# Performance work log

Measured on AMD Instinct MI355X. Metric: run time of the kernel, lower is better.

Reference implementation:

```python
import jax, jax.numpy as jnp
import numpy as np

NUM_CLASSES = 80
C_OUT = 81
SCORE_THR = 0.02
IOU_THR = 0.45
TOPK = 1000
IMG_MAX = 320.0
STRIDES = [16, 32, 64, 107, 160, 320]
MIN_SIZES = [48, 100, 150, 202, 253, 304]
MAX_SIZES = [100, 150, 202, 253, 304, 320]
FEAT = [20, 10, 5, 3, 2, 1]
MAX_RATIO = float(abs(np.log(0.016)))


def _base_anchors(level):
    base = float(MIN_SIZES[level])
    scales = np.array([1.0, np.sqrt(MAX_SIZES[level] / MIN_SIZES[level])])
    ratios = np.array([1.0, 0.5, 2.0, 1.0 / 3.0, 3.0])
    h_ratios = np.sqrt(ratios)
    w_ratios = 1.0 / h_ratios
    # scale_major=False: scales vary along rows
    ws = (base * scales[:, None] * w_ratios[None, :]).reshape(-1)
    hs = (base * scales[:, None] * h_ratios[None, :]).reshape(-1)
    c = STRIDES[level] / 2.0
    ba = np.stack([c - 0.5 * ws, c - 0.5 * hs, c + 0.5 * ws, c + 0.5 * hs], -1)
    return ba[[0, 5, 1, 2, 3, 4]]  # index_select reorder, 6 anchors/loc


def _priors(level):
    ba = _base_anchors(level)
    f, s = FEAT[level], STRIDES[level]
    sx = np.arange(f, dtype=np.float64) * s
    xx = np.tile(sx, f)
    yy = np.repeat(sx, f)
    shifts = np.stack([xx, yy, xx, yy], -1)  # [f*f,4]
    return (ba[None, :, :] + shifts[:, None, :]).reshape(-1, 4).astype(np.float32)


PRIORS = [jnp.asarray(_priors(i)) for i in range(6)]


def delta2bbox(priors, deltas):
    stds = jnp.array([0.1, 0.1, 0.2, 0.2], dtype=deltas.dtype)
    d = deltas * stds
    pxy = (priors[:, :2] + priors[:, 2:]) * 0.5
    pwh = priors[:, 2:] - priors[:, :2]
    dwh = jnp.clip(d[:, 2:], -MAX_RATIO, MAX_RATIO)
    gxy = pxy + pwh * d[:, :2]
    gwh = pwh * jnp.exp(dwh)
    boxes = jnp.concatenate([gxy - 0.5 * gwh, gxy + 0.5 * gwh], -1)
    return jnp.clip(boxes, 0.0, IMG_MAX)


def _nms_keep(boxes, valid, iou_thr):
    # greedy NMS over score-sorted boxes; returns bool keep mask
    K = boxes.shape[0]
    area = (boxes[:, 2] - boxes[:, 0]) * (boxes[:, 3] - boxes[:, 1])
    lt = jnp.maximum(boxes[:, None, :2], boxes[None, :, :2])
    rb = jnp.minimum(boxes[:, None, 2:], boxes[None, :, 2:])
    wh = jnp.clip(rb - lt, 0.0)
    inter = wh[..., 0] * wh[..., 1]
    iou = inter / (area[:, None] + area[None, :] - inter)
    ar = jnp.arange(K)

    def body(i, alive):
        sup = (iou[i] > iou_thr) & (ar > i) & alive[i]
        return alive & ~sup

    return jax.lax.fori_loop(0, K, body, valid)


def _single_image(cls_list, bb_list):
    boxes_l, scores_l, labels_l, valid_l = [], [], [], []
    for cls, bb, priors in zip(cls_list, bb_list, PRIORS):
        probs = jax.nn.softmax(cls.transpose(1, 2, 0).reshape(-1, C_OUT), axis=-1)[:, :NUM_CLASSES]
        flat = probs.reshape(-1)  # [N*80]
        k = min(TOPK, flat.shape[0])
        masked = jnp.where(flat > SCORE_THR, flat, -1.0)
        vals, idx = jax.lax.top_k(masked, k)
        valid = vals > SCORE_THR
        a_idx = idx // NUM_CLASSES
        lbl = idx % NUM_CLASSES
        deltas = bb.transpose(1, 2, 0).reshape(-1, 4)[a_idx]
        boxes = delta2bbox(priors[a_idx], deltas)
        boxes_l.append(boxes)
        scores_l.append(jnp.where(valid, vals, 0.0))
        labels_l.append(lbl)
        valid_l.append(valid)
    boxes = jnp.concatenate(boxes_l, 0)   # [K,4]
    scores = jnp.concatenate(scores_l, 0)
    labels = jnp.concatenate(labels_l, 0)
    valid = jnp.concatenate(valid_l, 0)

    # batched (class-aware) NMS via per-class coordinate offsets
    max_coord = boxes.max()
    offsets = labels.astype(boxes.dtype) * (max_coord + 1.0)
    boxes_nms = boxes + offsets[:, None]
    order = jnp.argsort(-jnp.where(valid, scores, -jnp.inf))
    boxes_s = boxes[order]
    scores_s = scores[order]
    labels_s = labels[order]
    valid_s = valid[order]
    keep = jax.lax.stop_gradient(
        _nms_keep(jax.lax.stop_gradient(boxes_nms[order]), valid_s, IOU_THR))
    dets = jnp.concatenate([boxes_s, scores_s[:, None]], -1) * keep[:, None].astype(boxes.dtype)
    return dets, labels_s, keep


def setup_inputs() -> dict:
    key = jax.random.key(0)
    ks = jax.random.split(key, 12)
    B = 4
    inp = {}
    for i, f in enumerate(FEAT):
        inp[f"cls{i}"] = jax.random.normal(ks[i], (B, 486, f, f), dtype=jnp.float32)
        inp[f"bb{i}"] = jax.random.normal(ks[6 + i], (B, 24, f, f), dtype=jnp.float32)
    return inp


def reference(cls0, cls1, cls2, cls3, cls4, cls5, bb0, bb1, bb2, bb3, bb4, bb5):
    def one(c0, c1, c2, c3, c4, c5, b0, b1, b2, b3, b4, b5):
        return _single_image([c0, c1, c2, c3, c4, c5], [b0, b1, b2, b3, b4, b5])
    dets, labels, keep = jax.vmap(one)(cls0, cls1, cls2, cls3, cls4, cls5,
                                       bb0, bb1, bb2, bb3, bb4, bb5)
    return dets, labels, keep
```

## Files before the change

kernel.cpp:

```cpp
#include <hip/hip_runtime.h>
#include <stdint.h>

#define NB 4
#define KTOT 5480
#define PER_IMG 258720
#define SCORE_THR 0.02f
#define IOU_THR 0.45f
#define REL_BASE 0x3CA3D70Bu
#define JCH 10
#define JSZ 548
#define ICH 11
#define NMSCAP 512

__constant__ int cFEAT[6]    = {20,10,5,3,2,1};
__constant__ int cSTRIDE[6]  = {16,32,64,107,160,320};
__constant__ int cMIN[6]     = {48,100,150,202,253,304};
__constant__ int cMAX[6]     = {100,150,202,253,304,320};
__constant__ int cNFLAT[6]   = {192000,48000,12000,4320,1920,480};
__constant__ int cFLATOFF[6] = {0,192000,240000,252000,256320,258240};
__constant__ int cKSEL[6]    = {1000,1000,1000,1000,1000,480};
__constant__ int cKOFF[6]    = {0,1000,2000,3000,4000,5000};
__constant__ double cRATIO[6] = {1.0,1.0,0.5,2.0,1.0/3.0,3.0};
__constant__ int eTLEV[14]   = {0,0,0,0,0,0,0,0,1,1,2,3,4,5};
__constant__ int eTCHK[14]   = {0,1,2,3,4,5,6,7,0,1,0,0,0,0};
__constant__ int eNCH[6]     = {8,2,1,1,1,1};

__device__ __forceinline__ unsigned long long mk_key(unsigned kb, int lev, unsigned idx) {
  return ((unsigned long long)kb << 21) |
         (unsigned long long)(0x1FFFFFu ^ (((unsigned)lev << 18) | idx));
}

__device__ __forceinline__ unsigned long long shfl64(unsigned long long x, int src) {
  int lo = __shfl((int)(unsigned)(x & 0xffffffffull), src);
  int hi = __shfl((int)(unsigned)(x >> 32), src);
  return ((unsigned long long)(unsigned)hi << 32) | (unsigned)lo;
}

__global__ __launch_bounds__(256) void k_softmax(
    const float* __restrict__ c0, const float* __restrict__ c1,
    const float* __restrict__ c2, const float* __restrict__ c3,
    const float* __restrict__ c4, const float* __restrict__ c5,
    float* __restrict__ scores, unsigned* __restrict__ ghist)
{
  int t = blockIdx.x;
  int b = t / 78, rem = t % 78;
  int lev, a, cb;
  if (rem < 42)      { lev = 0; a = rem / 7;        cb = (rem % 7) * 64; }
  else if (rem < 54) { lev = 1; a = (rem - 42) >> 1; cb = ((rem - 42) & 1) * 64; }
  else               { lev = 2 + (rem - 54) / 6; a = (rem - 54) % 6; cb = 0; }
  const float* cls = (lev==0)?c0:(lev==1)?c1:(lev==2)?c2:(lev==3)?c3:(lev==4)?c4:c5;
  int f = cFEAT[lev], ff = f * f;
  int ncell = ff - cb; if (ncell > 64) ncell = 64;

  __shared__ float tile[81 * 64];
  const float* base = cls + (size_t)(b * 486 + a * 81) * ff + cb;
  for (int t2 = threadIdx.x; t2 < 81 * 64; t2 += 256) {
    int c = t2 >> 6, cell = t2 & 63;
    if (cell < ncell)
      tile[(c << 6) | (cell ^ (c & 63))] = base[c * ff + cell];
  }
  __syncthreads();

  int lane = threadIdx.x & 63, w = threadIdx.x >> 6;
  unsigned* h = ghist + (size_t)(b * 6 + lev) * 8192;
  for (int cell = w; cell < ncell; cell += 4) {
    float v1 = tile[(lane << 6) | (cell ^ lane)];
    float v2 = (lane <= 16) ? tile[((lane + 64) << 6) | (cell ^ lane)]
                            : __uint_as_float(0xff800000u);
    float mx = fmaxf(v1, v2);
    #pragma unroll
    for (int m = 32; m; m >>= 1) mx = fmaxf(mx, __shfl_xor(mx, m));
    float e1 = expf(v1 - mx);
    float e2 = (lane <= 16) ? expf(v2 - mx) : 0.f;
    float sm = e1 + e2;
    #pragma unroll
    for (int m = 32; m; m >>= 1) sm += __shfl_xor(sm, m);
    int row = (cb + cell) * 6 + a;
    float* out = scores + (size_t)b * PER_IMG + cFLATOFF[lev] + row * 80;
    float p1 = e1 / sm;
    out[lane] = (p1 > SCORE_THR) ? p1 : -1.f;
    if (p1 > SCORE_THR)
      atomicAdd(&h[(__float_as_uint(p1) - REL_BASE) >> 13], 1u);
    if (lane < 16) {
      float p2 = e2 / sm;
      out[lane + 64] = (p2 > SCORE_THR) ? p2 : -1.f;
      if (p2 > SCORE_THR)
        atomicAdd(&h[(__float_as_uint(p2) - REL_BASE) >> 13], 1u);
    }
  }
}

__global__ __launch_bounds__(1024) void k_plan(
    const unsigned* __restrict__ ghist, unsigned* __restrict__ ctrl)
{
  int task = blockIdx.x;
  int lev = task % 6;
  int tid = threadIdx.x;
  if (lev == 5) { if (tid == 0) ctrl[task * 8] = 2u; return; }
  unsigned k = (unsigned)cKSEL[lev];
  const unsigned* h = ghist + (size_t)task * 8192;
  unsigned loc[8];
  unsigned ssum = 0;
  #pragma unroll
  for (int j = 0; j < 8; ++j) { loc[j] = h[tid * 8 + j]; ssum += loc[j]; }
  __shared__ unsigned sc[1024];
  sc[tid] = ssum;
  __syncthreads();
  for (int off = 1; off < 1024; off <<= 1) {
    unsigned cur = sc[tid];
    unsigned add = (tid + off < 1024) ? sc[tid + off] : 0u;
    __syncthreads();
    sc[tid] = cur + add;
    __syncthreads();
  }
  unsigned c = sc[0];
  if (c < k) { if (tid == 0) ctrl[task * 8] = 1u; return; }
  unsigned above = (tid == 1023) ? 0u : sc[tid + 1];
  unsigned run = above;
  #pragma unroll
  for (int j = 7; j >= 0; --j) {
    unsigned hj = loc[j];
    if (run < k && run + hj >= k) {
      ctrl[task * 8 + 0] = 0u;
      ctrl[task * 8 + 1] = (unsigned)(tid * 8 + j);
    }
    run += hj;
  }
}

__global__ __launch_bounds__(256) void k_emit2(
    const float* __restrict__ scores, unsigned* __restrict__ ctrl,
    unsigned long long* __restrict__ selkeys, unsigned long long* __restrict__ eqg)
{
  int b = blockIdx.x / 14, ent = blockIdx.x % 14;
  int lev = eTLEV[ent], chk = eTCHK[ent];
  int task = b * 6 + lev;
  int n = cNFLAT[lev];
  int tid = threadIdx.x;
  const float* s = scores + (size_t)b * PER_IMG + cFLATOFF[lev];
  unsigned long long* out = selkeys + (size_t)b * KTOT + cKOFF[lev];

  if (lev == 5) {
    for (int i = tid; i < n; i += 256) {
      float v = s[i];
      unsigned kb = (v > SCORE_THR) ? __float_as_uint(v) : 0u;
      out[i] = mk_key(kb, lev, (unsigned)i);
    }
    return;
  }

  __shared__ unsigned long long wbuf[1024];
  __shared__ unsigned long long ebuf[4096];
  __shared__ unsigned wcnt, ecnt, sbw, sbe;
  if (tid == 0) { wcnt = 0; ecnt = 0; }
  __syncthreads();

  unsigned mode = ctrl[task * 8];
  int csz = n / eNCH[lev];
  int start = chk * csz;
  const float4* s4 = (const float4*)(s + start);
  int n4 = csz >> 2;

  if (mode == 0u) {
    unsigned b1 = ctrl[task * 8 + 1];
    unsigned base_lo = REL_BASE + (b1 << 13);
    unsigned base_hi = base_lo + 8192u;
    #pragma unroll 4
    for (int i0 = tid; i0 < n4; i0 += 256) {
      float4 vv = s4[i0];
      #pragma unroll
      for (int e2 = 0; e2 < 4; ++e2) {
        float v = (e2==0)?vv.x:(e2==1)?vv.y:(e2==2)?vv.z:vv.w;
        if (v > SCORE_THR) {
          unsigned kb = __float_as_uint(v);
          unsigned idx = (unsigned)(start + i0 * 4 + e2);
          if (kb >= base_hi) {
            unsigned p = atomicAdd(&wcnt, 1u);
            if (p < 1024u) wbuf[p] = mk_key(kb, lev, idx);
          } else if (kb >= base_lo) {
            unsigned p = atomicAdd(&ecnt, 1u);
            if (p < 4096u) ebuf[p] = mk_key(kb, lev, idx);
          }
        }
      }
    }
  } else {
    #pragma unroll 4
    for (int i0 = tid; i0 < n4; i0 += 256) {
      float4 vv = s4[i0];
      #pragma unroll
      for (int e2 = 0; e2 < 4; ++e2) {
        float v = (e2==0)?vv.x:(e2==1)?vv.y:(e2==2)?vv.z:vv.w;
        if (v > SCORE_THR) {
          unsigned p = atomicAdd(&wcnt, 1u);
          if (p < 1024u) wbuf[p] = mk_key(__float_as_uint(v), lev,
                                          (unsigned)(start + i0 * 4 + e2));
        }
      }
    }
  }
  __syncthreads();
  if (tid == 0) {
    sbw = atomicAdd(&ctrl[task * 8 + 2], wcnt);
    sbe = atomicAdd(&ctrl[task * 8 + 3], ecnt);
  }
  __syncthreads();
  unsigned nw = (wcnt < 1024u) ? wcnt : 1024u;
  unsigned ne = (ecnt < 4096u) ? ecnt : 4096u;
  unsigned bw = sbw, be = sbe;
  for (unsigned t = tid; t < nw; t += 256) out[bw + t] = wbuf[t];
  for (unsigned t = tid; t < ne; t += 256) {
    unsigned g = be + t;
    if (g < 4096u) eqg[(size_t)task * 4096 + g] = ebuf[t];
  }
}

__global__ __launch_bounds__(1024) void k_finalize2(
    const float* __restrict__ scores, const unsigned* __restrict__ ctrl,
    unsigned long long* __restrict__ selkeys, const unsigned long long* __restrict__ eqg)
{
  int task = blockIdx.x;
  int b = task / 6, lev = task % 6;
  if (lev == 5) return;
  int tid = threadIdx.x;
  unsigned k = (unsigned)cKSEL[lev];
  int n = cNFLAT[lev];
  const float* s = scores + (size_t)b * PER_IMG + cFLATOFF[lev];
  unsigned long long* out = selkeys + (size_t)b * KTOT + cKOFF[lev];
  unsigned levtag = (unsigned)lev << 18;
  unsigned mode = ctrl[task * 8];

  __shared__ unsigned long long eqb[4096];
  __shared__ unsigned sc[1024];
  __shared__ unsigned sh_cnt, sh_eq, sh_byte, sh_r;

  if (mode == 0u) {
    unsigned cnt = ctrl[task * 8 + 2];
    unsigned e = ctrl[task * 8 + 3];
    unsigned need = k - cnt;
    if (e <= 4096u) {
      const unsigned long long* eq = eqg + (size_t)task * 4096;
      if (e == need) {
        for (unsigned t = tid; t < need; t += 1024) out[cnt + t] = eq[t];
        return;
      }
      unsigned P = 1; while (P < e) P <<= 1;
      for (unsigned t = tid; t < P; t += 1024) eqb[t] = (t < e) ? eq[t] : 0ull;
      __syncthreads();
      for (unsigned sz = 2; sz <= P; sz <<= 1)
        for (unsigned st = sz >> 1; st; st >>= 1) {
          for (unsigned w = tid; w < P / 2; w += 1024) {
            unsigned i = ((w & ~(st - 1)) << 1) | (w & (st - 1));
            unsigned l = i | st;
            bool up = ((i & sz) == 0);
            unsigned long long A = eqb[i], B = eqb[l];
            if ((A < B) == up) { eqb[i] = B; eqb[l] = A; }
          }
          __syncthreads();
        }
      for (unsigned t = tid; t < need; t += 1024) out[cnt + t] = eqb[t];
      return;
    }
  } else if (mode == 1u) {
    unsigned c = ctrl[task * 8 + 2];
    unsigned need = k - c;
    unsigned base = 0;
    for (int start = 0; start < n && base < need; start += 1024) {
      int i = start + tid;
      unsigned pred = (i < n && !(s[i] > SCORE_THR)) ? 1u : 0u;
      sc[tid] = pred;
      __syncthreads();
      for (int off = 1; off < 1024; off <<= 1) {
        unsigned add = (tid >= off) ? sc[tid - off] : 0u;
        unsigned v = sc[tid];
        __syncthreads();
        sc[tid] = v + add;
        __syncthreads();
      }
      unsigned incl = sc[tid];
      unsigned total = sc[1023];
      unsigned excl = incl - pred;
      if (pred && (base + excl) < need)
        out[c + base + excl] =
            (unsigned long long)(0x1FFFFFu ^ (levtag | (unsigned)i));
      __syncthreads();
      base += total;
    }
    return;
  }

  unsigned* hist = sc;
  unsigned* equ = (unsigned*)eqb;
  unsigned prefix = 0, r = k;
  for (int pass = 3; pass >= 0; --pass) {
    int shift = pass * 8;
    for (int i = tid; i < 256; i += 1024) hist[i] = 0;
    __syncthreads();
    for (int i = tid; i < n; i += 1024) {
      float v = s[i];
      unsigned kb = (v > SCORE_THR) ? __float_as_uint(v) : 0u;
      bool match = (pass == 3) || (((kb ^ prefix) >> (shift + 8)) == 0u);
      if (match) atomicAdd(&hist[(kb >> shift) & 255u], 1u);
    }
    __syncthreads();
    if (tid == 0) {
      unsigned cum = 0, byte = 0, rr = r;
      for (int bb = 255; bb >= 0; --bb) {
        unsigned hh = hist[bb];
        if (cum + hh >= r) { byte = (unsigned)bb; rr = r - cum; break; }
        cum += hh;
      }
      sh_byte = byte; sh_r = rr;
    }
    __syncthreads();
    prefix |= (sh_byte << shift);
    r = sh_r;
    __syncthreads();
  }
  unsigned Kstar = prefix;
  if (tid == 0) { sh_cnt = 0; sh_eq = 0; }
  __syncthreads();
  for (int i = tid; i < n; i += 1024) {
    float v = s[i];
    unsigned kb = (v > SCORE_THR) ? __float_as_uint(v) : 0u;
    if (kb > Kstar) {
      unsigned slot = atomicAdd(&sh_cnt, 1u);
      out[slot] = mk_key(kb, lev, (unsigned)i);
    } else if (kb == Kstar) {
      unsigned es = atomicAdd(&sh_eq, 1u);
      if (es < 4096u) equ[es] = (unsigned)i;
    }
  }
  __syncthreads();
  unsigned m = sh_cnt;
  unsigned e2 = (sh_eq < 4096u) ? sh_eq : 4096u;
  unsigned need2 = k - m;
  if (e2 > need2) {
    unsigned P = 1; while (P < e2) P <<= 1;
    for (unsigned t = tid; t < P; t += 1024) if (t >= e2) equ[t] = 0xFFFFFFFFu;
    __syncthreads();
    for (unsigned sz = 2; sz <= P; sz <<= 1)
      for (unsigned st = sz >> 1; st; st >>= 1) {
        for (unsigned w = tid; w < P / 2; w += 1024) {
          unsigned i = ((w & ~(st - 1)) << 1) | (w & (st - 1));
          unsigned l = i | st;
          bool up = ((i & sz) == 0);
          unsigned A = equ[i], B = equ[l];
          if ((A > B) == up) { equ[i] = B; equ[l] = A; }
        }
        __syncthreads();
      }
  }
  __syncthreads();
  for (unsigned t = tid; t < need2; t += 1024)
    out[m + t] = ((unsigned long long)Kstar << 21) |
                 (unsigned long long)(0x1FFFFFu ^ (levtag | equ[t]));
}

__global__ __launch_bounds__(512) void k_rank(
    const unsigned long long* __restrict__ selkeys, unsigned* __restrict__ rank_part)
{
  int blk = blockIdx.x;
  int jc = blk % JCH;
  int rest = blk / JCH;
  int ic = rest % ICH, b = rest / ICH;
  int tid = threadIdx.x;
  __shared__ __align__(16) unsigned long long sk[JSZ];
  const unsigned long long* keys = selkeys + (size_t)b * KTOT;
  for (int j = tid; j < JSZ; j += 512) sk[j] = keys[jc * JSZ + j];
  int i = ic * 512 + tid;
  unsigned long long mk = (i < KTOT) ? keys[i] : 0ull;
  __syncthreads();
  unsigned r = 0;
  const ulonglong2* sk2 = (const ulonglong2*)sk;
  #pragma unroll 8
  for (int j = 0; j < JSZ / 2; ++j) {
    ulonglong2 kk = sk2[j];
    r += (kk.x > mk) ? 1u : 0u;
    r += (kk.y > mk) ? 1u : 0u;
  }
  if (i < KTOT) rank_part[((size_t)jc * NB + b) * KTOT + i] = r;
}

__global__ __launch_bounds__(512) void k_decode(
    const unsigned long long* __restrict__ selkeys, const unsigned* __restrict__ rank_part,
    const float* __restrict__ g0, const float* __restrict__ g1,
    const float* __restrict__ g2, const float* __restrict__ g3,
    const float* __restrict__ g4, const float* __restrict__ g5,
    float* __restrict__ boxes, float* __restrict__ oscore,
    unsigned char* __restrict__ lab8, unsigned* __restrict__ obmax_u,
    float* __restrict__ outp)
{
  int b = blockIdx.x / ICH, ic = blockIdx.x % ICH;
  int tid = threadIdx.x;
  int i = ic * 512 + tid;
  __shared__ double ba[6][6][4];
  if (tid < 36) {
    int lev = tid / 6, a = tid % 6;
    double base = (double)cMIN[lev];
    double scl = (a == 1) ? sqrt((double)cMAX[lev] / (double)cMIN[lev]) : 1.0;
    double hr = sqrt(cRATIO[a]);
    double wr = 1.0 / hr;
    double wsz = base * scl * wr;
    double hsz = base * scl * hr;
    double cc = (double)cSTRIDE[lev] / 2.0;
    ba[lev][a][0] = cc - 0.5 * wsz;
    ba[lev][a][1] = cc - 0.5 * hsz;
    ba[lev][a][2] = cc + 0.5 * wsz;
    ba[lev][a][3] = cc + 0.5 * hsz;
  }
  __syncthreads();

  float lmax = 0.f;
  if (i < KTOT) {
    unsigned long long mk = selkeys[(size_t)b * KTOT + i];
    unsigned r = 0;
    #pragma unroll
    for (int jc = 0; jc < JCH; ++jc)
      r += rank_part[((size_t)jc * NB + b) * KTOT + i];
    unsigned tag = 0x1FFFFFu ^ (unsigned)(mk & 0x1FFFFFull);
    int lev = tag >> 18;
    int fi = tag & 0x3FFFF;
    unsigned vb2 = (unsigned)(mk >> 21);
    int valid = (vb2 != 0u);
    float score = valid ? __uint_as_float(vb2) : 0.f;
    int label = fi % 80;
    int arow = fi / 80;
    int a = arow % 6, cell = arow / 6;
    int f = cFEAT[lev], ff = f * f;
    int x = cell % f, y = cell / f;
    const float* gb = (lev==0)?g0:(lev==1)?g1:(lev==2)?g2:(lev==3)?g3:(lev==4)?g4:g5;
    const float* pb = gb + (size_t)(b * 24 + a * 4) * ff + y * f + x;
    float d0 = pb[0] * 0.1f, d1 = pb[ff] * 0.1f;
    float d2 = pb[2 * ff] * 0.2f, d3 = pb[3 * ff] * 0.2f;
    const float MR = (float)4.135166556742356;
    d2 = fminf(fmaxf(d2, -MR), MR);
    d3 = fminf(fmaxf(d3, -MR), MR);
    double shx = (double)(x * cSTRIDE[lev]);
    double shy = (double)(y * cSTRIDE[lev]);
    float p0 = (float)(ba[lev][a][0] + shx);
    float p1 = (float)(ba[lev][a][1] + shy);
    float p2 = (float)(ba[lev][a][2] + shx);
    float p3 = (float)(ba[lev][a][3] + shy);
    float pxc = (p0 + p2) * 0.5f, pyc = (p1 + p3) * 0.5f;
    float pw = p2 - p0, ph = p3 - p1;
    float gx = pxc + pw * d0, gy = pyc + ph * d1;
    float gw = pw * expf(d2), gh = ph * expf(d3);
    float x1 = gx - 0.5f * gw, y1 = gy - 0.5f * gh;
    float x2 = gx + 0.5f * gw, y2 = gy + 0.5f * gh;
    x1 = fminf(fmaxf(x1, 0.f), 320.f);
    y1 = fminf(fmaxf(y1, 0.f), 320.f);
    x2 = fminf(fmaxf(x2, 0.f), 320.f);
    y2 = fminf(fmaxf(y2, 0.f), 320.f);
    size_t o = (size_t)b * KTOT + (size_t)r;
    boxes[o * 4 + 0] = x1; boxes[o * 4 + 1] = y1;
    boxes[o * 4 + 2] = x2; boxes[o * 4 + 3] = y2;
    oscore[o] = score;
    lab8[o] = valid ? (unsigned char)label : (unsigned char)0xFF;
    outp[(size_t)NB * KTOT * 5 + o] = (float)label;
    if (!valid) {
      float* det = outp + o * 5;
      det[0] = 0.f; det[1] = 0.f; det[2] = 0.f; det[3] = 0.f; det[4] = 0.f;
      outp[(size_t)NB * KTOT * 6 + o] = 0.f;
    }
    lmax = fmaxf(fmaxf(x1, y1), fmaxf(x2, y2));
  }
  #pragma unroll
  for (int m = 32; m; m >>= 1) lmax = fmaxf(lmax, __shfl_xor(lmax, m));
  if ((tid & 63) == 0) atomicMax(&obmax_u[b], __float_as_uint(lmax));
}

__global__ __launch_bounds__(256) void k_nms(
    const float* __restrict__ boxes, const float* __restrict__ oscore,
    const unsigned char* __restrict__ lab8, const unsigned* __restrict__ obmax_u,
    float* __restrict__ out)
{
  int blk = blockIdx.x;
  int b = blk / 80, cls = blk % 80;
  int tid = threadIdx.x;
  int lane = tid & 63, w = tid >> 6;

  __shared__ unsigned short list[NMSCAP];
  __shared__ float ox1[NMSCAP], oy1[NMSCAP], ox2[NMSCAP], oy2[NMSCAP];
  __shared__ float oar[NMSCAP], osc[NMSCAP];
  __shared__ float rx1[NMSCAP], ry1[NMSCAP], rx2[NMSCAP], ry2[NMSCAP];
  __shared__ unsigned long long mask[NMSCAP][8];
  __shared__ unsigned ccnt[24], cbase[24];
  __shared__ int sh_n;
  __shared__ unsigned long long alive_s[8];

  float ofs = (float)cls * (__uint_as_float(obmax_u[b]) + 1.0f);
  const unsigned* lb32 = (const unsigned*)(lab8 + (size_t)b * KTOT);

  unsigned long long balA[6][4];
  #pragma unroll
  for (int ci = 0; ci < 6; ++ci) {
    int chunk = w + ci * 4;
    unsigned v = 0xFFFFFFFFu;
    if (chunk < 22) {
      int u = chunk * 64 + lane;
      if (u < KTOT / 4) v = lb32[u];
    }
    unsigned long long m0 = __ballot(((v      ) & 0xFFu) == (unsigned)cls);
    unsigned long long m1 = __ballot(((v >>  8) & 0xFFu) == (unsigned)cls);
    unsigned long long m2 = __ballot(((v >> 16) & 0xFFu) == (unsigned)cls);
    unsigned long long m3 = __ballot(((v >> 24) & 0xFFu) == (unsigned)cls);
    balA[ci][0] = m0; balA[ci][1] = m1; balA[ci][2] = m2; balA[ci][3] = m3;
    if (chunk < 22 && lane == 0)
      ccnt[chunk] = (unsigned)(__popcll(m0) + __popcll(m1) + __popcll(m2) + __popcll(m3));
  }
  __syncthreads();
  if (tid == 0) {
    unsigned tot = 0;
    for (int c = 0; c < 22; ++c) { cbase[c] = tot; tot += ccnt[c]; }
    sh_n = (tot < NMSCAP) ? (int)tot : NMSCAP;
  }
  __syncthreads();
  int n = sh_n;
  unsigned long long blt = (lane == 0) ? 0ull : ((~0ull) >> (64 - lane));
  #pragma unroll
  for (int ci = 0; ci < 6; ++ci) {
    int chunk = w + ci * 4;
    if (chunk < 22) {
      unsigned pos = cbase[chunk];
      unsigned below = (unsigned)(__popcll(balA[ci][0] & blt) + __popcll(balA[ci][1] & blt) +
                                  __popcll(balA[ci][2] & blt) + __popcll(balA[ci][3] & blt));
      unsigned within = 0;
      #pragma unroll
      for (int k = 0; k < 4; ++k) {
        if ((balA[ci][k] >> lane) & 1ull) {
          unsigned mypos = pos + below + within;
          if (mypos < NMSCAP) list[mypos] = (unsigned short)(chunk * 256 + lane * 4 + k);
          ++within;
        }
      }
    }
  }
  __syncthreads();

  for (int t = tid; t < n; t += 256) {
    int pos = list[t];
    size_t o = (size_t)b * KTOT + pos;
    float4 bb = *(const float4*)(boxes + o * 4);
    rx1[t] = bb.x; ry1[t] = bb.y; rx2[t] = bb.z; ry2[t] = bb.w;
    float a1 = bb.x + ofs, b1 = bb.y + ofs, a2 = bb.z + ofs, b2 = bb.w + ofs;
    ox1[t] = a1; oy1[t] = b1; ox2[t] = a2; oy2[t] = b2;
    oar[t] = (a2 - a1) * (b2 - b1);
    osc[t] = oscore[o];
  }
  __syncthreads();

  int nw = (n + 63) >> 6;
  for (int i = tid; i < n; i += 256) {
    float ax1 = ox1[i], ay1 = oy1[i], ax2 = ox2[i], ay2 = oy2[i], aar = oar[i];
    int w0 = i >> 6;
    for (int wd = w0; wd < nw; ++wd) {
      unsigned long long m = 0;
      int jbase = wd << 6;
      int jend = n - jbase; if (jend > 64) jend = 64;
      for (int jj = 0; jj < jend; ++jj) {
        int j = jbase + jj;
        if (j > i) {
          float ix1 = fmaxf(ax1, ox1[j]);
          float iy1 = fmaxf(ay1, oy1[j]);
          float ix2 = fminf(ax2, ox2[j]);
          float iy2 = fminf(ay2, oy2[j]);
          float iw = fmaxf(ix2 - ix1, 0.f);
          float ih = fmaxf(iy2 - iy1, 0.f);
          float inter = iw * ih;
          float iou = inter / (aar + oar[j] - inter);
          if (iou > IOU_THR) m |= (1ull << jj);
        }
      }
      mask[i][wd] = m;
    }
  }
  __syncthreads();

  if (w == 0) {
    unsigned long long aw = 0;
    if (lane < nw) {
      int rem = n - (lane << 6);
      aw = (rem >= 64) ? ~0ull : ((1ull << rem) - 1ull);
    }
    for (int i = 0; i < n; ++i) {
      int wi = i >> 6;
      unsigned long long mrow = (lane >= wi && lane < nw) ? mask[i][lane] : 0ull;
      unsigned long long tw = shfl64(aw, wi);
      if ((tw >> (i & 63)) & 1ull) aw &= ~mrow;
    }
    if (lane < 8) alive_s[lane] = aw;
  }
  __syncthreads();

  for (int t = tid; t < n; t += 256) {
    float kf = ((alive_s[t >> 6] >> (t & 63)) & 1ull) ? 1.f : 0.f;
    int pos = list[t];
    size_t o = (size_t)b * KTOT + pos;
    float* det = out + o * 5;
    det[0] = rx1[t] * kf; det[1] = ry1[t] * kf;
    det[2] = rx2[t] * kf; det[3] = ry2[t] * kf;
    det[4] = osc[t] * kf;
    out[(size_t)NB * KTOT * 6 + o] = kf;
  }
}

extern "C" void kernel_launch(void* const* d_in, const int* in_sizes, int n_in,
                              void* d_out, int out_size, void* d_ws, size_t ws_size,
                              hipStream_t stream) {
  (void)in_sizes; (void)n_in; (void)out_size; (void)ws_size;
  const float* cls[6]; const float* bbx[6];
  for (int i = 0; i < 6; ++i) {
    cls[i] = (const float*)d_in[2 * i];
    bbx[i] = (const float*)d_in[2 * i + 1];
  }
  char* ws = (char*)d_ws;
  float* scores = (float*)ws;
  unsigned* rank_part = (unsigned*)ws;
  unsigned long long* selkeys = (unsigned long long*)(ws + 4139520);
  float* boxes  = (float*)(ws + 4314880);
  float* oscore = (float*)(ws + 4665600);
  unsigned char* lab8 = (unsigned char*)(ws + 4753280);
  unsigned* obmax_u = (unsigned*)(ws + 5016320);
  unsigned* ghist = (unsigned*)(ws + 5016576);
  unsigned* ctrl  = (unsigned*)(ws + 5803008);
  unsigned long long* eqg = (unsigned long long*)(ws + 5803776);

  hipMemsetAsync(ws + 5016320, 0, 787456, stream);
  k_softmax<<<NB * 78, 256, 0, stream>>>(cls[0], cls[1], cls[2], cls[3], cls[4], cls[5],
                                         scores, ghist);
  k_plan<<<24, 1024, 0, stream>>>(ghist, ctrl);
  k_emit2<<<NB * 14, 256, 0, stream>>>(scores, ctrl, selkeys, eqg);
  k_finalize2<<<24, 1024, 0, stream>>>(scores, ctrl, selkeys, eqg);
  k_rank<<<NB * ICH * JCH, 512, 0, stream>>>(selkeys, rank_part);
  k_decode<<<NB * ICH, 512, 0, stream>>>(selkeys, rank_part, bbx[0], bbx[1], bbx[2],
                                         bbx[3], bbx[4], bbx[5], boxes, oscore, lab8,
                                         obmax_u, (float*)d_out);
  k_nms<<<NB * 80, 256, 0, stream>>>(boxes, oscore, lab8, obmax_u, (float*)d_out);
}
```

Baseline: 113.2 us.

## Fuse top-k selection into one kernel and merge rank with decode

New measurement: 224.0 us. 97.9% more time.

```diff
diff --git a/kernel.cpp b/kernel.cpp
--- a/kernel.cpp
+++ b/kernel.cpp
@@ -9,7 +9,7 @@
 #define REL_BASE 0x3CA3D70Bu
 #define JCH 10
 #define JSZ 548
-#define ICH 11
+#define ICH 22
 #define NMSCAP 512
 
 __constant__ int cFEAT[6]    = {20,10,5,3,2,1};
@@ -21,9 +21,6 @@
 __constant__ int cKSEL[6]    = {1000,1000,1000,1000,1000,480};
 __constant__ int cKOFF[6]    = {0,1000,2000,3000,4000,5000};
 __constant__ double cRATIO[6] = {1.0,1.0,0.5,2.0,1.0/3.0,3.0};
-__constant__ int eTLEV[14]   = {0,0,0,0,0,0,0,0,1,1,2,3,4,5};
-__constant__ int eTCHK[14]   = {0,1,2,3,4,5,6,7,0,1,0,0,0,0};
-__constant__ int eNCH[6]     = {8,2,1,1,1,1};
 
 __device__ __forceinline__ unsigned long long mk_key(unsigned kb, int lev, unsigned idx) {
   return ((unsigned long long)kb << 21) |
@@ -40,12 +37,12 @@
     const float* __restrict__ c0, const float* __restrict__ c1,
     const float* __restrict__ c2, const float* __restrict__ c3,
     const float* __restrict__ c4, const float* __restrict__ c5,
-    float* __restrict__ scores, unsigned* __restrict__ ghist)
+    float* __restrict__ scores)
 {
   int t = blockIdx.x;
   int b = t / 78, rem = t % 78;
   int lev, a, cb;
-  if (rem < 42)      { lev = 0; a = rem / 7;        cb = (rem % 7) * 64; }
+  if (rem < 42)      { lev = 0; a = rem / 7;         cb = (rem % 7) * 64; }
   else if (rem < 54) { lev = 1; a = (rem - 42) >> 1; cb = ((rem - 42) & 1) * 64; }
   else               { lev = 2 + (rem - 54) / 6; a = (rem - 54) % 6; cb = 0; }
   const float* cls = (lev==0)?c0:(lev==1)?c1:(lev==2)?c2:(lev==3)?c3:(lev==4)?c4:c5;
@@ -62,7 +59,6 @@
   __syncthreads();
 
   int lane = threadIdx.x & 63, w = threadIdx.x >> 6;
-  unsigned* h = ghist + (size_t)(b * 6 + lev) * 8192;
   for (int cell = w; cell < ncell; cell += 4) {
     float v1 = tile[(lane << 6) | (cell ^ lane)];
     float v2 = (lane <= 16) ? tile[((lane + 64) << 6) | (cell ^ lane)]
@@ -79,31 +75,63 @@
     float* out = scores + (size_t)b * PER_IMG + cFLATOFF[lev] + row * 80;
     float p1 = e1 / sm;
     out[lane] = (p1 > SCORE_THR) ? p1 : -1.f;
-    if (p1 > SCORE_THR)
-      atomicAdd(&h[(__float_as_uint(p1) - REL_BASE) >> 13], 1u);
     if (lane < 16) {
       float p2 = e2 / sm;
       out[lane + 64] = (p2 > SCORE_THR) ? p2 : -1.f;
-      if (p2 > SCORE_THR)
-        atomicAdd(&h[(__float_as_uint(p2) - REL_BASE) >> 13], 1u);
     }
   }
 }
 
-__global__ __launch_bounds__(1024) void k_plan(
-    const unsigned* __restrict__ ghist, unsigned* __restrict__ ctrl)
+__global__ __launch_bounds__(1024) void k_select(
+    const float* __restrict__ scores, unsigned long long* __restrict__ selkeys,
+    unsigned* __restrict__ obmax_done)
 {
   int task = blockIdx.x;
-  int lev = task % 6;
+  int b = task / 6, lev = task % 6;
   int tid = threadIdx.x;
-  if (lev == 5) { if (tid == 0) ctrl[task * 8] = 2u; return; }
+  int n = cNFLAT[lev];
   unsigned k = (unsigned)cKSEL[lev];
-  const unsigned* h = ghist + (size_t)task * 8192;
+  const float* s = scores + (size_t)b * PER_IMG + cFLATOFF[lev];
+  unsigned long long* out = selkeys + (size_t)b * KTOT + cKOFF[lev];
+  unsigned levtag = (unsigned)lev << 18;
+
+  if (task == 0 && tid < 92) obmax_done[tid] = 0;
+
+  if (lev == 5) {
+    for (int i = tid; i < n; i += 1024) {
+      float v = s[i];
+      unsigned kb = (v > SCORE_THR) ? __float_as_uint(v) : 0u;
+      out[i] = mk_key(kb, lev, (unsigned)i);
+    }
+    return;
+  }
+
+  __shared__ union { unsigned hist[8192]; unsigned long long eqb[4096]; } u;
+  __shared__ unsigned sc[1024];
+  __shared__ unsigned sh_cnt, sh_eq, sh_b1, sh_byte, sh_r;
+
+  for (int i = tid; i < 8192; i += 1024) u.hist[i] = 0;
+  __syncthreads();
+  {
+    const float4* s4 = (const float4*)s;
+    int n4 = n >> 2;
+    #pragma unroll 4
+    for (int i0 = tid; i0 < n4; i0 += 1024) {
+      float4 vv = s4[i0];
+      #pragma unroll
+      for (int e = 0; e < 4; ++e) {
+        float v = (e == 0) ? vv.x : (e == 1) ? vv.y : (e == 2) ? vv.z : vv.w;
+        if (v > SCORE_THR)
+          atomicAdd(&u.hist[(__float_as_uint(v) - REL_BASE) >> 13], 1u);
+      }
+    }
+  }
+  __syncthreads();
+
   unsigned loc[8];
   unsigned ssum = 0;
   #pragma unroll
-  for (int j = 0; j < 8; ++j) { loc[j] = h[tid * 8 + j]; ssum += loc[j]; }
-  __shared__ unsigned sc[1024];
+  for (int j = 0; j < 8; ++j) { loc[j] = u.hist[tid * 8 + j]; ssum += loc[j]; }
   sc[tid] = ssum;
   __syncthreads();
   for (int off = 1; off < 1024; off <<= 1) {
@@ -114,138 +142,121 @@
     __syncthreads();
   }
   unsigned c = sc[0];
-  if (c < k) { if (tid == 0) ctrl[task * 8] = 1u; return; }
-  unsigned above = (tid == 1023) ? 0u : sc[tid + 1];
-  unsigned run = above;
-  #pragma unroll
-  for (int j = 7; j >= 0; --j) {
-    unsigned hj = loc[j];
-    if (run < k && run + hj >= k) {
-      ctrl[task * 8 + 0] = 0u;
-      ctrl[task * 8 + 1] = (unsigned)(tid * 8 + j);
-    }
-    run += hj;
-  }
-}
-
-__global__ __launch_bounds__(256) void k_emit2(
-    const float* __restrict__ scores, unsigned* __restrict__ ctrl,
-    unsigned long long* __restrict__ selkeys, unsigned long long* __restrict__ eqg)
-{
-  int b = blockIdx.x / 14, ent = blockIdx.x % 14;
-  int lev = eTLEV[ent], chk = eTCHK[ent];
-  int task = b * 6 + lev;
-  int n = cNFLAT[lev];
-  int tid = threadIdx.x;
-  const float* s = scores + (size_t)b * PER_IMG + cFLATOFF[lev];
-  unsigned long long* out = selkeys + (size_t)b * KTOT + cKOFF[lev];
-
-  if (lev == 5) {
-    for (int i = tid; i < n; i += 256) {
+
+  if (c >= k) {
+    unsigned above = (tid == 1023) ? 0u : sc[tid + 1];
+    unsigned run = above;
+    #pragma unroll
+    for (int j = 7; j >= 0; --j) {
+      unsigned hj = loc[j];
+      if (run < k && run + hj >= k) sh_b1 = (unsigned)(tid * 8 + j);
+      run += hj;
+    }
+    if (tid == 0) { sh_cnt = 0; sh_eq = 0; }
+    __syncthreads();
+    unsigned b1 = sh_b1;
+    unsigned base_lo = REL_BASE + (b1 << 13);
+    unsigned base_hi = base_lo + 8192u;
+
+    {
+      const float4* s4 = (const float4*)s;
+      int n4 = n >> 2;
+      #pragma unroll 4
+      for (int i0 = tid; i0 < n4; i0 += 1024) {
+        float4 vv = s4[i0];
+        #pragma unroll
+        for (int e = 0; e < 4; ++e) {
+          float v = (e == 0) ? vv.x : (e == 1) ? vv.y : (e == 2) ? vv.z : vv.w;
+          if (v > SCORE_THR) {
+            unsigned kb = __float_as_uint(v);
+            unsigned idx = (unsigned)(i0 * 4 + e);
+            if (kb >= base_hi) {
+              unsigned slot = atomicAdd(&sh_cnt, 1u);
+              out[slot] = mk_key(kb, lev, idx);
+            } else if (kb >= base_lo) {
+              unsigned p = atomicAdd(&sh_eq, 1u);
+              if (p < 4096u) u.eqb[p] = mk_key(kb, lev, idx);
+            }
+          }
+        }
+      }
+    }
+    __syncthreads();
+    unsigned cnt = sh_cnt;
+    unsigned e = sh_eq;
+    unsigned need = k - cnt;
+    if (e <= 4096u) {
+      if (e == need) {
+        for (unsigned t = tid; t < need; t += 1024) out[cnt + t] = u.eqb[t];
+      } else {
+        unsigned P = 1; while (P < e) P <<= 1;
+        for (unsigned t = tid; t < P; t += 1024) if (t >= e) u.eqb[t] = 0ull;
+        __syncthreads();
+        for (unsigned sz = 2; sz <= P; sz <<= 1)
+          for (unsigned st = sz >> 1; st; st >>= 1) {
+            for (unsigned w = tid; w < P / 2; w += 1024) {
+              unsigned i = ((w & ~(st - 1)) << 1) | (w & (st - 1));
+              unsigned l = i | st;
+              bool up = ((i & sz) == 0);
+              unsigned long long A = u.eqb[i], B = u.eqb[l];
+              if ((A < B) == up) { u.eqb[i] = B; u.eqb[l] = A; }
+            }
+            __syncthreads();
+          }
+        for (unsigned t = tid; t < need; t += 1024) out[cnt + t] = u.eqb[t];
+      }
+      return;
+    }
+
+    unsigned* hist = sc;
+    unsigned* equ = (unsigned*)u.eqb;
+    unsigned prefix = 0, r = k;
+    for (int pass = 3; pass >= 0; --pass) {
+      int shift = pass * 8;
+      for (int i = tid; i < 256; i += 1024) hist[i] = 0;
+      __syncthreads();
+      for (int i = tid; i < n; i += 1024) {
+        float v = s[i];
+        unsigned kb = (v > SCORE_THR) ? __float_as_uint(v) : 0u;
+        bool match = (pass == 3) || (((kb ^ prefix) >> (shift + 8)) == 0u);
+        if (match) atomicAdd(&hist[(kb >> shift) & 255u], 1u);
+      }
+      __syncthreads();
+      if (tid == 0) {
+        unsigned cum = 0, byte = 0, rr = r;
+        for (int bb = 255; bb >= 0; --bb) {
+          unsigned hh = hist[bb];
+          if (cum + hh >= r) { byte = (unsigned)bb; rr = r - cum; break; }
+          cum += hh;
+        }
+        sh_byte = byte; sh_r = rr;
+      }
+      __syncthreads();
+      prefix |= (sh_byte << shift);
+      r = sh_r;
+      __syncthreads();
+    }
+    unsigned Kstar = prefix;
+    if (tid == 0) { sh_cnt = 0; sh_eq = 0; }
+    __syncthreads();
+    for (int i = tid; i < n; i += 1024) {
       float v = s[i];
       unsigned kb = (v > SCORE_THR) ? __float_as_uint(v) : 0u;
-      out[i] = mk_key(kb, lev, (unsigned)i);
-    }
-    return;
-  }
-
-  __shared__ unsigned long long wbuf[1024];
-  __shared__ unsigned long long ebuf[4096];
-  __shared__ unsigned wcnt, ecnt, sbw, sbe;
-  if (tid == 0) { wcnt = 0; ecnt = 0; }
-  __syncthreads();
-
-  unsigned mode = ctrl[task * 8];
-  int csz = n / eNCH[lev];
-  int start = chk * csz;
-  const float4* s4 = (const float4*)(s + start);
-  int n4 = csz >> 2;
-
-  if (mode == 0u) {
-    unsigned b1 = ctrl[task * 8 + 1];
-    unsigned base_lo = REL_BASE + (b1 << 13);
-    unsigned base_hi = base_lo + 8192u;
-    #pragma unroll 4
-    for (int i0 = tid; i0 < n4; i0 += 256) {
-      float4 vv = s4[i0];
-      #pragma unroll
-      for (int e2 = 0; e2 < 4; ++e2) {
-        float v = (e2==0)?vv.x:(e2==1)?vv.y:(e2==2)?vv.z:vv.w;
-        if (v > SCORE_THR) {
-          unsigned kb = __float_as_uint(v);
-          unsigned idx = (unsigned)(start + i0 * 4 + e2);
-          if (kb >= base_hi) {
-            unsigned p = atomicAdd(&wcnt, 1u);
-            if (p < 1024u) wbuf[p] = mk_key(kb, lev, idx);
-          } else if (kb >= base_lo) {
-            unsigned p = atomicAdd(&ecnt, 1u);
-            if (p < 4096u) ebuf[p] = mk_key(kb, lev, idx);
-          }
-        }
-      }
-    }
-  } else {
-    #pragma unroll 4
-    for (int i0 = tid; i0 < n4; i0 += 256) {
-      float4 vv = s4[i0];
-      #pragma unroll
-      for (int e2 = 0; e2 < 4; ++e2) {
-        float v = (e2==0)?vv.x:(e2==1)?vv.y:(e2==2)?vv.z:vv.w;
-        if (v > SCORE_THR) {
-          unsigned p = atomicAdd(&wcnt, 1u);
-          if (p < 1024u) wbuf[p] = mk_key(__float_as_uint(v), lev,
-                                          (unsigned)(start + i0 * 4 + e2));
-        }
-      }
-    }
-  }
-  __syncthreads();
-  if (tid == 0) {
-    sbw = atomicAdd(&ctrl[task * 8 + 2], wcnt);
-    sbe = atomicAdd(&ctrl[task * 8 + 3], ecnt);
-  }
-  __syncthreads();
-  unsigned nw = (wcnt < 1024u) ? wcnt : 1024u;
-  unsigned ne = (ecnt < 4096u) ? ecnt : 4096u;
-  unsigned bw = sbw, be = sbe;
-  for (unsigned t = tid; t < nw; t += 256) out[bw + t] = wbuf[t];
-  for (unsigned t = tid; t < ne; t += 256) {
-    unsigned g = be + t;
-    if (g < 4096u) eqg[(size_t)task * 4096 + g] = ebuf[t];
-  }
-}
-
-__global__ __launch_bounds__(1024) void k_finalize2(
-    const float* __restrict__ scores, const unsigned* __restrict__ ctrl,
-    unsigned long long* __restrict__ selkeys, const unsigned long long* __restrict__ eqg)
-{
-  int task = blockIdx.x;
-  int b = task / 6, lev = task % 6;
-  if (lev == 5) return;
-  int tid = threadIdx.x;
-  unsigned k = (unsigned)cKSEL[lev];
-  int n = cNFLAT[lev];
-  const float* s = scores + (size_t)b * PER_IMG + cFLATOFF[lev];
-  unsigned long long* out = selkeys + (size_t)b * KTOT + cKOFF[lev];
-  unsigned levtag = (unsigned)lev << 18;
-  unsigned mode = ctrl[task * 8];
-
-  __shared__ unsigned long long eqb[4096];
-  __shared__ unsigned sc[1024];
-  __shared__ unsigned sh_cnt, sh_eq, sh_byte, sh_r;
-
-  if (mode == 0u) {
-    unsigned cnt = ctrl[task * 8 + 2];
-    unsigned e = ctrl[task * 8 + 3];
-    unsigned need = k - cnt;
-    if (e <= 4096u) {
-      const unsigned long long* eq = eqg + (size_t)task * 4096;
-      if (e == need) {
-        for (unsigned t = tid; t < need; t += 1024) out[cnt + t] = eq[t];
-        return;
-      }
-      unsigned P = 1; while (P < e) P <<= 1;
-      for (unsigned t = tid; t < P; t += 1024) eqb[t] = (t < e) ? eq[t] : 0ull;
+      if (kb > Kstar) {
+        unsigned slot = atomicAdd(&sh_cnt, 1u);
+        out[slot] = mk_key(kb, lev, (unsigned)i);
+      } else if (kb == Kstar) {
+        unsigned es = atomicAdd(&sh_eq, 1u);
+        if (es < 4096u) equ[es] = (unsigned)i;
+      }
+    }
+    __syncthreads();
+    unsigned m = sh_cnt;
+    unsigned e2 = (sh_eq < 4096u) ? sh_eq : 4096u;
+    unsigned need2 = k - m;
+    if (e2 > need2) {
+      unsigned P = 1; while (P < e2) P <<= 1;
+      for (unsigned t = tid; t < P; t += 1024) if (t >= e2) equ[t] = 0xFFFFFFFFu;
       __syncthreads();
       for (unsigned sz = 2; sz <= P; sz <<= 1)
         for (unsigned st = sz >> 1; st; st >>= 1) {
@@ -253,148 +264,106 @@
             unsigned i = ((w & ~(st - 1)) << 1) | (w & (st - 1));
             unsigned l = i | st;
             bool up = ((i & sz) == 0);
-            unsigned long long A = eqb[i], B = eqb[l];
-            if ((A < B) == up) { eqb[i] = B; eqb[l] = A; }
+            unsigned A = equ[i], B = equ[l];
+            if ((A > B) == up) { equ[i] = B; equ[l] = A; }
           }
           __syncthreads();
         }
-      for (unsigned t = tid; t < need; t += 1024) out[cnt + t] = eqb[t];
-      return;
-    }
-  } else if (mode == 1u) {
-    unsigned c = ctrl[task * 8 + 2];
-    unsigned need = k - c;
-    unsigned base = 0;
-    for (int start = 0; start < n && base < need; start += 1024) {
-      int i = start + tid;
-      unsigned pred = (i < n && !(s[i] > SCORE_THR)) ? 1u : 0u;
-      sc[tid] = pred;
+    }
+    __syncthreads();
+    for (unsigned t = tid; t < need2; t += 1024)
+      out[m + t] = ((unsigned long long)Kstar << 21) |
+                   (unsigned long long)(0x1FFFFFu ^ (levtag | equ[t]));
+    return;
+  }
+
+  if (tid == 0) sh_cnt = 0;
+  __syncthreads();
+  {
+    const float4* s4 = (const float4*)s;
+    int n4 = n >> 2;
+    #pragma unroll 4
+    for (int i0 = tid; i0 < n4; i0 += 1024) {
+      float4 vv = s4[i0];
+      #pragma unroll
+      for (int e = 0; e < 4; ++e) {
+        float v = (e == 0) ? vv.x : (e == 1) ? vv.y : (e == 2) ? vv.z : vv.w;
+        if (v > SCORE_THR) {
+          unsigned slot = atomicAdd(&sh_cnt, 1u);
+          out[slot] = mk_key(__float_as_uint(v), lev, (unsigned)(i0 * 4 + e));
+        }
+      }
+    }
+  }
+  __syncthreads();
+  unsigned need = k - c;
+  unsigned base = 0;
+  for (int start = 0; start < n && base < need; start += 1024) {
+    int i = start + tid;
+    unsigned pred = (i < n && !(s[i] > SCORE_THR)) ? 1u : 0u;
+    sc[tid] = pred;
+    __syncthreads();
+    for (int off = 1; off < 1024; off <<= 1) {
+      unsigned add = (tid >= off) ? sc[tid - off] : 0u;
+      unsigned v = sc[tid];
       __syncthreads();
-      for (int off = 1; off < 1024; off <<= 1) {
-        unsigned add = (tid >= off) ? sc[tid - off] : 0u;
-        unsigned v = sc[tid];
-        __syncthreads();
-        sc[tid] = v + add;
-        __syncthreads();
-      }
-      unsigned incl = sc[tid];
-      unsigned total = sc[1023];
-      unsigned excl = incl - pred;
-      if (pred && (base + excl) < need)
-        out[c + base + excl] =
-            (unsigned long long)(0x1FFFFFu ^ (levtag | (unsigned)i));
+      sc[tid] = v + add;
       __syncthreads();
-      base += total;
-    }
-    return;
-  }
-
-  unsigned* hist = sc;
-  unsigned* equ = (unsigned*)eqb;
-  unsigned prefix = 0, r = k;
-  for (int pass = 3; pass >= 0; --pass) {
-    int shift = pass * 8;
-    for (int i = tid; i < 256; i += 1024) hist[i] = 0;
-    __syncthreads();
-    for (int i = tid; i < n; i += 1024) {
-      float v = s[i];
-      unsigned kb = (v > SCORE_THR) ? __float_as_uint(v) : 0u;
-      bool match = (pass == 3) || (((kb ^ prefix) >> (shift + 8)) == 0u);
-      if (match) atomicAdd(&hist[(kb >> shift) & 255u], 1u);
-    }
-    __syncthreads();
-    if (tid == 0) {
-      unsigned cum = 0, byte = 0, rr = r;
-      for (int bb = 255; bb >= 0; --bb) {
-        unsigned hh = hist[bb];
-        if (cum + hh >= r) { byte = (unsigned)bb; rr = r - cum; break; }
-        cum += hh;
-      }
-      sh_byte = byte; sh_r = rr;
-    }
-    __syncthreads();
-    prefix |= (sh_byte << shift);
-    r = sh_r;
-    __syncthreads();
-  }
-  unsigned Kstar = prefix;
-  if (tid == 0) { sh_cnt = 0; sh_eq = 0; }
-  __syncthreads();
-  for (int i = tid; i < n; i += 1024) {
-    float v = s[i];
-    unsigned kb = (v > SCORE_THR) ? __float_as_uint(v) : 0u;
-    if (kb > Kstar) {
-      unsigned slot = atomicAdd(&sh_cnt, 1u);
-      out[slot] = mk_key(kb, lev, (unsigned)i);
-    } else if (kb == Kstar) {
-      unsigned es = atomicAdd(&sh_eq, 1u);
-      if (es < 4096u) equ[es] = (unsigned)i;
-    }
-  }
-  __syncthreads();
-  unsigned m = sh_cnt;
-  unsigned e2 = (sh_eq < 4096u) ? sh_eq : 4096u;
-  unsigned need2 = k - m;
-  if (e2 > need2) {
-    unsigned P = 1; while (P < e2) P <<= 1;
-    for (unsigned t = tid; t < P; t += 1024) if (t >= e2) equ[t] = 0xFFFFFFFFu;
-    __syncthreads();
-    for (unsigned sz = 2; sz <= P; sz <<= 1)
-      for (unsigned st = sz >> 1; st; st >>= 1) {
-        for (unsigned w = tid; w < P / 2; w += 1024) {
-          unsigned i = ((w & ~(st - 1)) << 1) | (w & (st - 1));
-          unsigned l = i | st;
-          bool up = ((i & sz) == 0);
-          unsigned A = equ[i], B = equ[l];
-          if ((A > B) == up) { equ[i] = B; equ[l] = A; }
-        }
-        __syncthreads();
-      }
-  }
-  __syncthreads();
-  for (unsigned t = tid; t < need2; t += 1024)
-    out[m + t] = ((unsigned long long)Kstar << 21) |
-                 (unsigned long long)(0x1FFFFFu ^ (levtag | equ[t]));
+    }
+    unsigned incl = sc[tid];
+    unsigned total = sc[1023];
+    unsigned excl = incl - pred;
+    if (pred && (base + excl) < need)
+      out[c + base + excl] =
+          (unsigned long long)(0x1FFFFFu ^ (levtag | (unsigned)i));
+    __syncthreads();
+    base += total;
+  }
 }
 
-__global__ __launch_bounds__(512) void k_rank(
-    const unsigned long long* __restrict__ selkeys, unsigned* __restrict__ rank_part)
+__global__ __launch_bounds__(256) void k_rankdec(
+    const unsigned long long* __restrict__ selkeys, unsigned* rank_part,
+    const float* __restrict__ g0, const float* __restrict__ g1,
+    const float* __restrict__ g2, const float* __restrict__ g3,
+    const float* __restrict__ g4, const float* __restrict__ g5,
+    float* __restrict__ boxes, float* __restrict__ oscore,
+    unsigned char* __restrict__ lab8, unsigned* obmax_done,
+    float* __restrict__ outp)
 {
   int blk = blockIdx.x;
   int jc = blk % JCH;
-  int rest = blk / JCH;
-  int ic = rest % ICH, b = rest / ICH;
+  int g = blk / JCH;
+  int ic = g % ICH, b = g / ICH;
   int tid = threadIdx.x;
+  int i = ic * 256 + tid;
+
   __shared__ __align__(16) unsigned long long sk[JSZ];
+  __shared__ double ba[6][6][4];
+  __shared__ int slast;
+
   const unsigned long long* keys = selkeys + (size_t)b * KTOT;
-  for (int j = tid; j < JSZ; j += 512) sk[j] = keys[jc * JSZ + j];
-  int i = ic * 512 + tid;
+  for (int j = tid; j < JSZ; j += 256) sk[j] = keys[jc * JSZ + j];
   unsigned long long mk = (i < KTOT) ? keys[i] : 0ull;
   __syncthreads();
-  unsigned r = 0;
+  unsigned rpart = 0;
   const ulonglong2* sk2 = (const ulonglong2*)sk;
   #pragma unroll 8
   for (int j = 0; j < JSZ / 2; ++j) {
     ulonglong2 kk = sk2[j];
-    r += (kk.x > mk) ? 1u : 0u;
-    r += (kk.y > mk) ? 1u : 0u;
-  }
-  if (i < KTOT) rank_part[((size_t)jc * NB + b) * KTOT + i] = r;
-}
-
-__global__ __launch_bounds__(512) void k_decode(
-    const unsigned long long* __restrict__ selkeys, const unsigned* __restrict__ rank_part,
-    const float* __restrict__ g0, const float* __restrict__ g1,
-    const float* __restrict__ g2, const float* __restrict__ g3,
-    const float* __restrict__ g4, const float* __restrict__ g5,
-    float* __restrict__ boxes, float* __restrict__ oscore,
-    unsigned char* __restrict__ lab8, unsigned* __restrict__ obmax_u,
-    float* __restrict__ outp)
-{
-  int b = blockIdx.x / ICH, ic = blockIdx.x % ICH;
-  int tid = threadIdx.x;
-  int i = ic * 512 + tid;
-  __shared__ double ba[6][6][4];
+    rpart += (kk.x > mk) ? 1u : 0u;
+    rpart += (kk.y > mk) ? 1u : 0u;
+  }
+  if (i < KTOT) rank_part[((size_t)jc * NB + b) * KTOT + i] = rpart;
+
+  __threadfence();
+  if (tid == 0) {
+    unsigned ret = atomicAdd(&obmax_done[4 + g], 1u);
+    slast = (ret == JCH - 1);
+  }
+  __syncthreads();
+  if (!slast) return;
+  __threadfence();
+
   if (tid < 36) {
     int lev = tid / 6, a = tid % 6;
     double base = (double)cMIN[lev];
@@ -413,11 +382,10 @@
 
   float lmax = 0.f;
   if (i < KTOT) {
-    unsigned long long mk = selkeys[(size_t)b * KTOT + i];
     unsigned r = 0;
     #pragma unroll
-    for (int jc = 0; jc < JCH; ++jc)
-      r += rank_part[((size_t)jc * NB + b) * KTOT + i];
+    for (int jc2 = 0; jc2 < JCH; ++jc2)
+      r += rank_part[((size_t)jc2 * NB + b) * KTOT + i];
     unsigned tag = 0x1FFFFFu ^ (unsigned)(mk & 0x1FFFFFull);
     int lev = tag >> 18;
     int fi = tag & 0x3FFFF;
@@ -467,12 +435,12 @@
   }
   #pragma unroll
   for (int m = 32; m; m >>= 1) lmax = fmaxf(lmax, __shfl_xor(lmax, m));
-  if ((tid & 63) == 0) atomicMax(&obmax_u[b], __float_as_uint(lmax));
+  if ((tid & 63) == 0) atomicMax(&obmax_done[b], __float_as_uint(lmax));
 }
 
 __global__ __launch_bounds__(256) void k_nms(
     const float* __restrict__ boxes, const float* __restrict__ oscore,
-    const unsigned char* __restrict__ lab8, const unsigned* __restrict__ obmax_u,
+    const unsigned char* __restrict__ lab8, const unsigned* __restrict__ obmax_done,
     float* __restrict__ out)
 {
   int blk = blockIdx.x;
@@ -489,7 +457,7 @@
   __shared__ int sh_n;
   __shared__ unsigned long long alive_s[8];
 
-  float ofs = (float)cls * (__uint_as_float(obmax_u[b]) + 1.0f);
+  float ofs = (float)cls * (__uint_as_float(obmax_done[b]) + 1.0f);
   const unsigned* lb32 = (const unsigned*)(lab8 + (size_t)b * KTOT);
 
   unsigned long long balA[6][4];
@@ -621,20 +589,13 @@
   float* boxes  = (float*)(ws + 4314880);
   float* oscore = (float*)(ws + 4665600);
   unsigned char* lab8 = (unsigned char*)(ws + 4753280);
-  unsigned* obmax_u = (unsigned*)(ws + 5016320);
-  unsigned* ghist = (unsigned*)(ws + 5016576);
-  unsigned* ctrl  = (unsigned*)(ws + 5803008);
-  unsigned long long* eqg = (unsigned long long*)(ws + 5803776);
-
-  hipMemsetAsync(ws + 5016320, 0, 787456, stream);
+  unsigned* obmax_done = (unsigned*)(ws + 5016320);
+
   k_softmax<<<NB * 78, 256, 0, stream>>>(cls[0], cls[1], cls[2], cls[3], cls[4], cls[5],
-                                         scores, ghist);
-  k_plan<<<24, 1024, 0, stream>>>(ghist, ctrl);
-  k_emit2<<<NB * 14, 256, 0, stream>>>(scores, ctrl, selkeys, eqg);
-  k_finalize2<<<24, 1024, 0, stream>>>(scores, ctrl, selkeys, eqg);
-  k_rank<<<NB * ICH * JCH, 512, 0, stream>>>(selkeys, rank_part);
-  k_decode<<<NB * ICH, 512, 0, stream>>>(selkeys, rank_part, bbx[0], bbx[1], bbx[2],
-                                         bbx[3], bbx[4], bbx[5], boxes, oscore, lab8,
-                                         obmax_u, (float*)d_out);
-  k_nms<<<NB * 80, 256, 0, stream>>>(boxes, oscore, lab8, obmax_u, (float*)d_out);
+                                         scores);
+  k_select<<<NB * 6, 1024, 0, stream>>>(scores, selkeys, obmax_done);
+  k_rankdec<<<NB * ICH * JCH, 256, 0, stream>>>(selkeys, rank_part, bbx[0], bbx[1],
+                                                bbx[2], bbx[3], bbx[4], bbx[5], boxes,
+                                                oscore, lab8, obmax_done, (float*)d_out);
+  k_nms<<<NB * 80, 256, 0, stream>>>(boxes, oscore, lab8, obmax_done, (float*)d_out);
 }
```
